# Optimization experiments

Hardware: AMD Instinct MI355X
Metric: run time of the kernel (lower is better)

Reference implementation:

```python
import jax, jax.numpy as jnp
import numpy as np

B, MQ, MK = 8, 512, 2048
Q_DIM, KV_DIM = 1024, 256
H = 8
QKC, VC = 1024, 1024
DQ, DV = QKC // H, VC // H
EPS = 1e-5  # nn.LayerNorm default


def _layer_norm(x, w, b):
    m = jnp.mean(x, axis=-1, keepdims=True)
    v = jnp.var(x, axis=-1, keepdims=True)
    return (x - m) * jax.lax.rsqrt(v + EPS) * w + b


def setup_inputs() -> dict:
    key = jax.random.key(0)
    ks = jax.random.split(key, 12)
    hidden_states = jax.random.normal(ks[0], (B, MQ, Q_DIM), dtype=jnp.float32)
    inputs = jax.random.normal(ks[1], (B, MK, KV_DIM), dtype=jnp.float32)
    # ragged per-batch kv lengths -> prefix-valid mask (matches keys[i, :n] packing)
    lengths = jax.random.randint(ks[2], (B,), MK // 4, MK + 1)
    inputs_mask = (jnp.arange(MK)[None, :] < lengths[:, None]).astype(jnp.int32)
    s = 0.02
    return {
        "hidden_states": hidden_states,
        "inputs": inputs,
        "inputs_mask": inputs_mask,
        "ln1_w": jnp.ones((Q_DIM,), jnp.float32),
        "ln1_b": jnp.zeros((Q_DIM,), jnp.float32),
        "ln2_w": jnp.ones((KV_DIM,), jnp.float32),
        "ln2_b": jnp.zeros((KV_DIM,), jnp.float32),
        "Wq": s * jax.random.normal(ks[3], (Q_DIM, QKC), dtype=jnp.float32),
        "bq": jnp.zeros((QKC,), jnp.float32),
        "Wk": s * jax.random.normal(ks[4], (KV_DIM, QKC), dtype=jnp.float32),
        "bk": jnp.zeros((QKC,), jnp.float32),
        "Wv": s * jax.random.normal(ks[5], (KV_DIM, VC), dtype=jnp.float32),
        "bv": jnp.zeros((VC,), jnp.float32),
    }


def reference(hidden_states, inputs, inputs_mask, ln1_w, ln1_b, ln2_w, ln2_b,
              Wq, bq, Wk, bk, Wv, bv):
    hs = _layer_norm(hidden_states, ln1_w, ln1_b)      # [B, MQ, Q_DIM]
    kv = _layer_norm(inputs, ln2_w, ln2_b)             # [B, MK, KV_DIM]

    q = (hs @ Wq + bq).reshape(B, MQ, H, DQ)           # [B, MQ, H, DQ]
    k = (kv @ Wk + bk).reshape(B, MK, H, DQ)           # [B, MK, H, DQ]
    v = (kv @ Wv + bv).reshape(B, MK, H, DV)           # [B, MK, H, DV]

    scores = jnp.einsum("bqhd,bkhd->bhqk", q, k) / jnp.sqrt(jnp.float32(DQ))
    mask_f = inputs_mask.astype(scores.dtype)          # [B, MK]
    neg = jnp.finfo(scores.dtype).min
    scores = scores + (1.0 - mask_f)[:, None, None, :] * neg
    probs = jax.nn.softmax(scores, axis=-1)            # [B, H, MQ, MK]

    ctx = jnp.einsum("bhqk,bkhd->bqhd", probs, v)      # [B, MQ, H, DV]
    return ctx.reshape(B, MQ, H * DV)
```

## Files before the change

kernel.cpp:

```cpp
#include <hip/hip_runtime.h>

#define DI __device__ __forceinline__

typedef _Float16 f16x8 __attribute__((ext_vector_type(8)));
typedef _Float16 f16x4 __attribute__((ext_vector_type(4)));
typedef float    f32x4 __attribute__((ext_vector_type(4)));

namespace {

constexpr int kB  = 8;
constexpr int kMQ = 512;
constexpr int kMK = 2048;
constexpr int kQKC = 1024;
constexpr int kVC  = 1024;

DI void gload16(const void* g, void* l) {
  __builtin_amdgcn_global_load_lds(
      (const __attribute__((address_space(1))) void*)g,
      (__attribute__((address_space(3))) void*)l, 16, 0, 0);
}

DI f32x4 mfma16(f16x8 a, f16x8 b, f32x4 c) {
  return __builtin_amdgcn_mfma_f32_16x16x32_f16(a, b, c, 0, 0, 0);
}

DI f32x4 mfma16k16(f16x4 a, f16x4 b, f32x4 c) {
  return __builtin_amdgcn_mfma_f32_16x16x16f16(a, b, c, 0, 0, 0);
}

template<int K, int N>
DI void transpose_dev(const float* __restrict__ W, _Float16* __restrict__ WT,
                      int bid, float (*t)[65]) {
  int nt = bid % (N / 64), kt = bid / (N / 64);
  int k0 = kt * 64, n0 = nt * 64;
  int tid = threadIdx.x;
#pragma unroll
  for (int j = 0; j < 16; ++j) {
    int e = tid + j * 256;
    int r = e >> 6, c = e & 63;
    t[r][c] = W[(size_t)(k0 + r) * N + n0 + c];
  }
  __syncthreads();
#pragma unroll
  for (int j = 0; j < 16; ++j) {
    int e = tid + j * 256;
    int r = e >> 6, c = e & 63;
    WT[(size_t)(n0 + r) * K + k0 + c] = (_Float16)t[c][r];
  }
}

DI void ln1024_dev(const float* __restrict__ x, const float* __restrict__ w,
                   const float* __restrict__ bb, _Float16* __restrict__ y,
                   int row, float* red) {
  int tid = threadIdx.x;
  const float4* xr = (const float4*)(x + (size_t)row * 1024);
  float4 v = xr[tid];
  float s = v.x + v.y + v.z + v.w;
  float q = v.x * v.x + v.y * v.y + v.z * v.z + v.w * v.w;
#pragma unroll
  for (int m = 32; m; m >>= 1) { s += __shfl_xor(s, m); q += __shfl_xor(q, m); }
  if ((tid & 63) == 0) { red[tid >> 6] = s; red[4 + (tid >> 6)] = q; }
  __syncthreads();
  s = red[0] + red[1] + red[2] + red[3];
  q = red[4] + red[5] + red[6] + red[7];
  float mean = s * (1.0f / 1024.0f);
  float var = q * (1.0f / 1024.0f) - mean * mean;
  float inv = rsqrtf(var + 1e-5f);
  f16x4 o;
  const float* wp = w + tid * 4;
  const float* bp = bb + tid * 4;
  o[0] = (_Float16)((v.x - mean) * inv * wp[0] + bp[0]);
  o[1] = (_Float16)((v.y - mean) * inv * wp[1] + bp[1]);
  o[2] = (_Float16)((v.z - mean) * inv * wp[2] + bp[2]);
  o[3] = (_Float16)((v.w - mean) * inv * wp[3] + bp[3]);
  *(f16x4*)(y + (size_t)row * 1024 + tid * 4) = o;
}

DI void ln256_dev(const float* __restrict__ x, const float* __restrict__ w,
                  const float* __restrict__ bb, _Float16* __restrict__ y, int bid) {
  int tid = threadIdx.x;
  int lane = tid & 63, wv = tid >> 6;
  size_t row = (size_t)bid * 4 + wv;
  const float4* xr = (const float4*)(x + row * 256);
  float4 v = xr[lane];
  float s = v.x + v.y + v.z + v.w;
  float q = v.x * v.x + v.y * v.y + v.z * v.z + v.w * v.w;
#pragma unroll
  for (int m = 32; m; m >>= 1) { s += __shfl_xor(s, m); q += __shfl_xor(q, m); }
  float mean = s * (1.0f / 256.0f);
  float var = q * (1.0f / 256.0f) - mean * mean;
  float inv = rsqrtf(var + 1e-5f);
  f16x4 o;
  const float* wp = w + lane * 4;
  const float* bp = bb + lane * 4;
  o[0] = (_Float16)((v.x - mean) * inv * wp[0] + bp[0]);
  o[1] = (_Float16)((v.y - mean) * inv * wp[1] + bp[1]);
  o[2] = (_Float16)((v.z - mean) * inv * wp[2] + bp[2]);
  o[3] = (_Float16)((v.w - mean) * inv * wp[3] + bp[3]);
  *(f16x4*)(y + row * 256 + lane * 4) = o;
}

__global__ __launch_bounds__(256) void prep_all(
    const float* __restrict__ Wq, const float* __restrict__ Wk, const float* __restrict__ Wv,
    _Float16* __restrict__ WqT, _Float16* __restrict__ WkT, _Float16* __restrict__ WvT,
    const float* __restrict__ hs, const float* __restrict__ ln1w, const float* __restrict__ ln1b,
    _Float16* __restrict__ hsln,
    const float* __restrict__ xin, const float* __restrict__ ln2w, const float* __restrict__ ln2b,
    _Float16* __restrict__ kvln) {
  __shared__ float tbuf[64][65];
  int bid = blockIdx.x;
  if (bid < 256) {
    transpose_dev<1024, 1024>(Wq, WqT, bid, tbuf);
  } else if (bid < 320) {
    transpose_dev<256, 1024>(Wk, WkT, bid - 256, tbuf);
  } else if (bid < 384) {
    transpose_dev<256, 1024>(Wv, WvT, bid - 320, tbuf);
  } else if (bid < 4480) {
    ln1024_dev(hs, ln1w, ln1b, hsln, bid - 384, (float*)tbuf);
  } else {
    ln256_dev(xin, ln2w, ln2b, kvln, bid - 4480);
  }
}

template<int M, int N, int K, bool BIAS_ROW, int MMODE, bool CM>
DI void gemm_dev(const _Float16* __restrict__ A, const _Float16* __restrict__ Bt,
                 const float* __restrict__ bias, const int* __restrict__ msk,
                 _Float16* __restrict__ C, int bid,
                 _Float16 (*As)[128 * 64], _Float16 (*Bs)[128 * 64]) {
  int tid = threadIdx.x, lane = tid & 63;
  int w = tid >> 6, wr = w >> 1, wc = w & 1;
  constexpr int NT = N / 128;
  constexpr int MT = M / 128;
  constexpr int KT = K / 64;
  int mt, nt;
  if constexpr (CM) { mt = bid % MT; nt = bid / MT; }
  else              { mt = bid / NT; nt = bid % NT; }
  if constexpr (MMODE == 1) { if (msk[mt * 128] == 0) return; }
  if constexpr (MMODE == 2) { if (msk[nt * 128] == 0) return; }
  const int l15 = lane & 15, l4 = lane >> 4;

  f32x4 acc[4][4] = {};

  const int rS = tid >> 3;
  const int cpS = tid & 7;

  auto stage = [&](int kt, int bufi) {
#pragma unroll
    for (int j = 0; j < 4; ++j) {
      int rr = rS + j * 32;
      int cg = cpS ^ (rr & 7);
      gload16(A  + ((size_t)(mt * 128 + rr) * K + kt * 64 + cg * 8),
              (char*)As[bufi] + j * 4096 + tid * 16);
      gload16(Bt + ((size_t)(nt * 128 + rr) * K + kt * 64 + cg * 8),
              (char*)Bs[bufi] + j * 4096 + tid * 16);
    }
  };

  stage(0, 0);
  __syncthreads();

  for (int kt = 0; kt < KT; ++kt) {
    int cur = kt & 1;
    if (kt + 1 < KT) stage(kt + 1, cur ^ 1);
#pragma unroll
    for (int ss = 0; ss < 2; ++ss) {
      f16x8 a[4], b[4];
#pragma unroll
      for (int m = 0; m < 4; ++m) {
        int ra = wr * 64 + m * 16 + l15;
        int cl = ss * 4 + l4;
        a[m] = *(const f16x8*)((const char*)As[cur] + ra * 128 + ((cl ^ (ra & 7)) << 4));
        int rb = wc * 64 + m * 16 + l15;
        b[m] = *(const f16x8*)((const char*)Bs[cur] + rb * 128 + ((cl ^ (rb & 7)) << 4));
      }
#pragma unroll
      for (int m = 0; m < 4; ++m)
#pragma unroll
        for (int n = 0; n < 4; ++n)
          acc[m][n] = mfma16(a[m], b[n], acc[m][n]);
    }
    __syncthreads();
  }

#pragma unroll
  for (int m = 0; m < 4; ++m) {
#pragma unroll
    for (int n = 0; n < 4; ++n) {
      int gi0 = mt * 128 + wr * 64 + m * 16 + l4 * 4;
      int gj  = nt * 128 + wc * 64 + n * 16 + l15;
#pragma unroll
      for (int r = 0; r < 4; ++r) {
        int gi = gi0 + r;
        float v = acc[m][n][r] + (BIAS_ROW ? bias[gi] : bias[gj]);
        C[(size_t)gi * N + gj] = (_Float16)v;
      }
    }
  }
}

__global__ __launch_bounds__(256) void gemm_all(
    const _Float16* __restrict__ hsln, const _Float16* __restrict__ WqT,
    const float* __restrict__ bq, _Float16* __restrict__ qbf,
    const _Float16* __restrict__ kvln, const _Float16* __restrict__ WkT,
    const float* __restrict__ bk, _Float16* __restrict__ kbf,
    const _Float16* __restrict__ WvT, const float* __restrict__ bv,
    _Float16* __restrict__ vT, const int* __restrict__ msk) {
  __shared__ _Float16 As[2][128 * 64];
  __shared__ _Float16 Bs[2][128 * 64];
  int bid = blockIdx.x;
  if (bid < 256) {
    gemm_dev<4096, 1024, 1024, false, 0, true>(hsln, WqT, bq, nullptr, qbf, bid, As, Bs);
  } else if (bid < 1280) {
    gemm_dev<16384, 1024, 256, false, 1, true>(kvln, WkT, bk, msk, kbf, bid - 256, As, Bs);
  } else {
    gemm_dev<1024, 16384, 256, true, 2, false>(WvT, kvln, bv, msk, vT, bid - 1280, As, Bs);
  }
}

__global__ __launch_bounds__(512, 4) void attn_kernel(const _Float16* __restrict__ qm,
                                                      const _Float16* __restrict__ km,
                                                      const _Float16* __restrict__ vT,
                                                      const int* __restrict__ msk,
                                                      float* __restrict__ out) {
  __shared__ _Float16 Ks[2][64 * 128];
  __shared__ _Float16 Vst[2][128 * 64];
  __shared__ float mlbuf[64][2];

  int tid = threadIdx.x, lane = tid & 63, w = tid >> 6;
  int bh = blockIdx.x & 63, qt = blockIdx.x >> 6;
  int h = bh & 7, b = bh >> 3;
  const int l15 = lane & 15, l4 = lane >> 4;
  const int wq = w & 3;
  const int g  = w >> 2;

  int vld = (lane < 32) ? msk[b * kMK + lane * 64] : 0;
  int ntiles = __popcll(__ballot(vld != 0));
  int lv = msk[b * kMK + (ntiles - 1) * 64 + lane];
  int lastlen = __popcll(__ballot(lv != 0));

  f16x8 qf[4];
#pragma unroll
  for (int kc = 0; kc < 4; ++kc)
    qf[kc] = *(const f16x8*)(qm +
        (size_t)(b * kMQ + qt * 64 + wq * 16 + l15) * kQKC +
        h * 128 + kc * 32 + l4 * 8);

  f32x4 o[8] = {};
  float rm = -1e30f, rl = 0.0f;

  const float sl2 = 0.08838834764831845f * 1.4426950408889634f;

  const int rK = tid >> 4, cpK = tid & 15;
  const int rV = tid >> 3, cpV = tid & 7;

  auto stage = [&](int kt, int bufi) {
#pragma unroll
    for (int j = 0; j < 2; ++j) {
      int rr = rK + j * 32;
      int cg = cpK ^ (rr & 7);
      gload16(km + (size_t)(b * kMK + kt * 64 + rr) * kQKC + h * 128 + cg * 8,
              (char*)Ks[bufi] + j * 8192 + tid * 16);
    }
#pragma unroll
    for (int j = 0; j < 2; ++j) {
      int dv = rV + j * 64;
      int cg = cpV ^ (dv & 7);
      gload16(vT + (size_t)(h * 128 + dv) * (kB * kMK) + (size_t)b * kMK + kt * 64 + cg * 8,
              (char*)Vst[bufi] + j * 8192 + tid * 16);
    }
  };

  stage(0, 0);
  __syncthreads();

  for (int kt = 0; kt < ntiles; ++kt) {
    int cur = kt & 1;
    if (kt + 1 < ntiles) stage(kt + 1, cur ^ 1);

    f32x4 sc[2] = {};
    __builtin_amdgcn_s_setprio(1);
#pragma unroll
    for (int kc = 0; kc < 4; ++kc) {
      f16x8 kb[2];
#pragma unroll
      for (int kf = 0; kf < 2; ++kf) {
        int rr = g * 32 + kf * 16 + l15;
        int cl = kc * 4 + l4;
        kb[kf] = *(const f16x8*)((const char*)Ks[cur] + rr * 256 + ((cl ^ (rr & 7)) << 4));
      }
#pragma unroll
      for (int kf = 0; kf < 2; ++kf)
        sc[kf] = mfma16(kb[kf], qf[kc], sc[kf]);
    }
    __builtin_amdgcn_s_setprio(0);

    if (kt == ntiles - 1) {
#pragma unroll
      for (int kf = 0; kf < 2; ++kf)
#pragma unroll
        for (int r = 0; r < 4; ++r)
          if (g * 32 + kf * 16 + l4 * 4 + r >= lastlen) sc[kf][r] = -3e38f;
    }

    float mx = sc[0][0];
#pragma unroll
    for (int kf = 0; kf < 2; ++kf)
#pragma unroll
      for (int r = 0; r < 4; ++r) mx = fmaxf(mx, sc[kf][r]);
    mx = fmaxf(mx, __shfl_xor(mx, 16));
    mx = fmaxf(mx, __shfl_xor(mx, 32));
    float al = 1.0f;
    if (__any(mx > rm)) {
      float nm = fmaxf(rm, mx);
      al = __builtin_amdgcn_exp2f((rm - nm) * sl2);
      rm = nm;
#pragma unroll
      for (int n = 0; n < 8; ++n)
#pragma unroll
        for (int r = 0; r < 4; ++r) o[n][r] *= al;
    }
    float nms = rm * sl2;
    float ts = 0.0f;
#pragma unroll
    for (int kf = 0; kf < 2; ++kf)
#pragma unroll
      for (int r = 0; r < 4; ++r) {
        float p = __builtin_amdgcn_exp2f(sc[kf][r] * sl2 - nms);
        sc[kf][r] = p;
        ts += p;
      }
    ts += __shfl_xor(ts, 16);
    ts += __shfl_xor(ts, 32);
    rl = rl * al + ts;

    f16x4 pb[2];
#pragma unroll
    for (int kf = 0; kf < 2; ++kf)
#pragma unroll
      for (int r = 0; r < 4; ++r) pb[kf][r] = (_Float16)sc[kf][r];

    __builtin_amdgcn_s_setprio(1);
#pragma unroll
    for (int n = 0; n < 8; ++n) {
      int dv = n * 16 + l15;
#pragma unroll
      for (int kf = 0; kf < 2; ++kf) {
        int phys = (g * 4 + kf * 2 + (l4 >> 1)) ^ (dv & 7);
        f16x4 vb = *(const f16x4*)((const char*)Vst[cur] +
                                   dv * 128 + (phys << 4) + (l4 & 1) * 8);
        o[n] = mfma16k16(vb, pb[kf], o[n]);
      }
    }
    __builtin_amdgcn_s_setprio(0);
    __syncthreads();
  }

  float* Mbuf = (float*)Ks;
  if (g == 1) {
#pragma unroll
    for (int n = 0; n < 8; ++n)
#pragma unroll
      for (int r = 0; r < 4; ++r)
        Mbuf[(n * 16 + l4 * 4 + r) * 64 + wq * 16 + l15] = o[n][r];
    if (l4 == 0) {
      mlbuf[wq * 16 + l15][0] = rm;
      mlbuf[wq * 16 + l15][1] = rl;
    }
  }
  __syncthreads();
  if (g == 1) return;

  float m1 = mlbuf[wq * 16 + l15][0];
  float l1 = mlbuf[wq * 16 + l15][1];
  float m = fmaxf(rm, m1);
  float w0 = __builtin_amdgcn_exp2f((rm - m) * sl2);
  float w1 = __builtin_amdgcn_exp2f((m1 - m) * sl2);
  float inv = 1.0f / (rl * w0 + l1 * w1);
  w0 *= inv; w1 *= inv;

  int qg = qt * 64 + wq * 16 + l15;
#pragma unroll
  for (int n = 0; n < 8; ++n) {
    f32x4 ov;
#pragma unroll
    for (int r = 0; r < 4; ++r) {
      float o1 = Mbuf[(n * 16 + l4 * 4 + r) * 64 + wq * 16 + l15];
      ov[r] = o[n][r] * w0 + o1 * w1;
    }
    *(f32x4*)(out + ((size_t)b * kMQ + qg) * kVC + h * 128 + n * 16 + l4 * 4) = ov;
  }
}

}

extern "C" void kernel_launch(void* const* d_in, const int* in_sizes, int n_in,
                              void* d_out, int out_size, void* d_ws, size_t ws_size,
                              hipStream_t stream) {
  (void)in_sizes; (void)n_in; (void)out_size; (void)ws_size;
  const float* hs   = (const float*)d_in[0];
  const float* xin  = (const float*)d_in[1];
  const int*   msk  = (const int*)d_in[2];
  const float* ln1w = (const float*)d_in[3];
  const float* ln1b = (const float*)d_in[4];
  const float* ln2w = (const float*)d_in[5];
  const float* ln2b = (const float*)d_in[6];
  const float* Wq   = (const float*)d_in[7];
  const float* bq   = (const float*)d_in[8];
  const float* Wk   = (const float*)d_in[9];
  const float* bk   = (const float*)d_in[10];
  const float* Wv   = (const float*)d_in[11];
  const float* bv   = (const float*)d_in[12];
  float* out = (float*)d_out;

  char* ws = (char*)d_ws;
  _Float16* qbf  = (_Float16*)(ws + 0);
  _Float16* kbf  = (_Float16*)(ws + 8388608);
  _Float16* vT   = (_Float16*)(ws + 41943040);
  _Float16* hsln = (_Float16*)(ws + 75497472);
  _Float16* kvln = (_Float16*)(ws + 83886080);
  _Float16* WqT  = (_Float16*)(ws + 92274688);
  _Float16* WkT  = (_Float16*)(ws + 94371840);
  _Float16* WvT  = (_Float16*)(ws + 94896128);

  prep_all<<<8576, 256, 0, stream>>>(Wq, Wk, Wv, WqT, WkT, WvT,
                                     hs, ln1w, ln1b, hsln,
                                     xin, ln2w, ln2b, kvln);
  gemm_all<<<2304, 256, 0, stream>>>(hsln, WqT, bq, qbf,
                                     kvln, WkT, bk, kbf,
                                     WvT, bv, vT, msk);
  attn_kernel<<<512, 512, 0, stream>>>(qbf, kbf, vT, msk, out);
}
```

Before: 122.0 us.

## Process two 16-row query fragments per wave to reuse K/V tiles

Each attention block now handles 128 query rows instead of 64, with every wave holding two query fragments and running two sets of MFMAs against each K and V fragment read from shared memory. This halves the total K/V global traffic and LDS reads per output, and halves the grid to 256 blocks. In exchange it doubles the accumulator registers, lowers the occupancy bound to 2 blocks per CU, and leaves fewer blocks than the device's CU count, which risks idle CUs and a worse load balance across ragged kv lengths.

Measured after the change: 116.2 us. 1.05x faster.

```diff
diff --git a/kernel.cpp b/kernel.cpp
--- a/kernel.cpp
+++ b/kernel.cpp
@@ -217,14 +217,15 @@
   }
 }
 
-__global__ __launch_bounds__(512, 4) void attn_kernel(const _Float16* __restrict__ qm,
+__global__ __launch_bounds__(512, 2) void attn_kernel(const _Float16* __restrict__ qm,
                                                       const _Float16* __restrict__ km,
                                                       const _Float16* __restrict__ vT,
                                                       const int* __restrict__ msk,
                                                       float* __restrict__ out) {
-  __shared__ _Float16 Ks[2][64 * 128];
-  __shared__ _Float16 Vst[2][128 * 64];
-  __shared__ float mlbuf[64][2];
+  __shared__ __align__(16) char smem[66560];
+  _Float16* Ksp = (_Float16*)smem;
+  _Float16* Vsp = (_Float16*)(smem + 32768);
+  float*    mlb = (float*)(smem + 65536);
 
   int tid = threadIdx.x, lane = tid & 63, w = tid >> 6;
   int bh = blockIdx.x & 63, qt = blockIdx.x >> 6;
@@ -238,15 +239,17 @@
   int lv = msk[b * kMK + (ntiles - 1) * 64 + lane];
   int lastlen = __popcll(__ballot(lv != 0));
 
-  f16x8 qf[4];
-#pragma unroll
-  for (int kc = 0; kc < 4; ++kc)
-    qf[kc] = *(const f16x8*)(qm +
-        (size_t)(b * kMQ + qt * 64 + wq * 16 + l15) * kQKC +
-        h * 128 + kc * 32 + l4 * 8);
-
-  f32x4 o[8] = {};
-  float rm = -1e30f, rl = 0.0f;
+  f16x8 qf[2][4];
+#pragma unroll
+  for (int m = 0; m < 2; ++m)
+#pragma unroll
+    for (int kc = 0; kc < 4; ++kc)
+      qf[m][kc] = *(const f16x8*)(qm +
+          (size_t)(b * kMQ + qt * 128 + wq * 32 + m * 16 + l15) * kQKC +
+          h * 128 + kc * 32 + l4 * 8);
+
+  f32x4 o[2][8] = {};
+  float rm[2] = {-1e30f, -1e30f}, rl[2] = {0.0f, 0.0f};
 
   const float sl2 = 0.08838834764831845f * 1.4426950408889634f;
 
@@ -259,14 +262,14 @@
       int rr = rK + j * 32;
       int cg = cpK ^ (rr & 7);
       gload16(km + (size_t)(b * kMK + kt * 64 + rr) * kQKC + h * 128 + cg * 8,
-              (char*)Ks[bufi] + j * 8192 + tid * 16);
+              (char*)Ksp + bufi * 16384 + j * 8192 + tid * 16);
     }
 #pragma unroll
     for (int j = 0; j < 2; ++j) {
       int dv = rV + j * 64;
       int cg = cpV ^ (dv & 7);
       gload16(vT + (size_t)(h * 128 + dv) * (kB * kMK) + (size_t)b * kMK + kt * 64 + cg * 8,
-              (char*)Vst[bufi] + j * 8192 + tid * 16);
+              (char*)Vsp + bufi * 16384 + j * 8192 + tid * 16);
     }
   };
 
@@ -277,7 +280,7 @@
     int cur = kt & 1;
     if (kt + 1 < ntiles) stage(kt + 1, cur ^ 1);
 
-    f32x4 sc[2] = {};
+    f32x4 sc[2][2] = {};
     __builtin_amdgcn_s_setprio(1);
 #pragma unroll
     for (int kc = 0; kc < 4; ++kc) {
@@ -286,58 +289,70 @@
       for (int kf = 0; kf < 2; ++kf) {
         int rr = g * 32 + kf * 16 + l15;
         int cl = kc * 4 + l4;
-        kb[kf] = *(const f16x8*)((const char*)Ks[cur] + rr * 256 + ((cl ^ (rr & 7)) << 4));
-      }
+        kb[kf] = *(const f16x8*)((const char*)Ksp + cur * 16384 + rr * 256 +
+                                 ((cl ^ (rr & 7)) << 4));
+      }
+#pragma unroll
+      for (int m = 0; m < 2; ++m)
+#pragma unroll
+        for (int kf = 0; kf < 2; ++kf)
+          sc[m][kf] = mfma16(kb[kf], qf[m][kc], sc[m][kf]);
+    }
+    __builtin_amdgcn_s_setprio(0);
+
+    if (kt == ntiles - 1) {
 #pragma unroll
       for (int kf = 0; kf < 2; ++kf)
-        sc[kf] = mfma16(kb[kf], qf[kc], sc[kf]);
-    }
-    __builtin_amdgcn_s_setprio(0);
-
-    if (kt == ntiles - 1) {
+#pragma unroll
+        for (int r = 0; r < 4; ++r)
+          if (g * 32 + kf * 16 + l4 * 4 + r >= lastlen) {
+            sc[0][kf][r] = -3e38f;
+            sc[1][kf][r] = -3e38f;
+          }
+    }
+
+    float mx[2];
+#pragma unroll
+    for (int m = 0; m < 2; ++m) {
+      float v = sc[m][0][0];
 #pragma unroll
       for (int kf = 0; kf < 2; ++kf)
 #pragma unroll
-        for (int r = 0; r < 4; ++r)
-          if (g * 32 + kf * 16 + l4 * 4 + r >= lastlen) sc[kf][r] = -3e38f;
-    }
-
-    float mx = sc[0][0];
-#pragma unroll
-    for (int kf = 0; kf < 2; ++kf)
-#pragma unroll
-      for (int r = 0; r < 4; ++r) mx = fmaxf(mx, sc[kf][r]);
-    mx = fmaxf(mx, __shfl_xor(mx, 16));
-    mx = fmaxf(mx, __shfl_xor(mx, 32));
-    float al = 1.0f;
-    if (__any(mx > rm)) {
-      float nm = fmaxf(rm, mx);
-      al = __builtin_amdgcn_exp2f((rm - nm) * sl2);
-      rm = nm;
-#pragma unroll
-      for (int n = 0; n < 8; ++n)
-#pragma unroll
-        for (int r = 0; r < 4; ++r) o[n][r] *= al;
-    }
-    float nms = rm * sl2;
-    float ts = 0.0f;
-#pragma unroll
-    for (int kf = 0; kf < 2; ++kf)
-#pragma unroll
-      for (int r = 0; r < 4; ++r) {
-        float p = __builtin_amdgcn_exp2f(sc[kf][r] * sl2 - nms);
-        sc[kf][r] = p;
-        ts += p;
-      }
-    ts += __shfl_xor(ts, 16);
-    ts += __shfl_xor(ts, 32);
-    rl = rl * al + ts;
-
-    f16x4 pb[2];
-#pragma unroll
-    for (int kf = 0; kf < 2; ++kf)
-#pragma unroll
-      for (int r = 0; r < 4; ++r) pb[kf][r] = (_Float16)sc[kf][r];
+        for (int r = 0; r < 4; ++r) v = fmaxf(v, sc[m][kf][r]);
+      v = fmaxf(v, __shfl_xor(v, 16));
+      v = fmaxf(v, __shfl_xor(v, 32));
+      mx[m] = v;
+    }
+    float al[2] = {1.0f, 1.0f};
+    if (__any(mx[0] > rm[0] || mx[1] > rm[1])) {
+#pragma unroll
+      for (int m = 0; m < 2; ++m) {
+        float nm = fmaxf(rm[m], mx[m]);
+        al[m] = __builtin_amdgcn_exp2f((rm[m] - nm) * sl2);
+        rm[m] = nm;
+#pragma unroll
+        for (int n = 0; n < 8; ++n)
+#pragma unroll
+          for (int r = 0; r < 4; ++r) o[m][n][r] *= al[m];
+      }
+    }
+    f16x4 pb[2][2];
+#pragma unroll
+    for (int m = 0; m < 2; ++m) {
+      float nms = rm[m] * sl2;
+      float ts = 0.0f;
+#pragma unroll
+      for (int kf = 0; kf < 2; ++kf)
+#pragma unroll
+        for (int r = 0; r < 4; ++r) {
+          float p = __builtin_amdgcn_exp2f(sc[m][kf][r] * sl2 - nms);
+          pb[m][kf][r] = (_Float16)p;
+          ts += p;
+        }
+      ts += __shfl_xor(ts, 16);
+      ts += __shfl_xor(ts, 32);
+      rl[m] = rl[m] * al[m] + ts;
+    }
 
     __builtin_amdgcn_s_setprio(1);
 #pragma unroll
@@ -346,48 +361,56 @@
 #pragma unroll
       for (int kf = 0; kf < 2; ++kf) {
         int phys = (g * 4 + kf * 2 + (l4 >> 1)) ^ (dv & 7);
-        f16x4 vb = *(const f16x4*)((const char*)Vst[cur] +
+        f16x4 vb = *(const f16x4*)((const char*)Vsp + cur * 16384 +
                                    dv * 128 + (phys << 4) + (l4 & 1) * 8);
-        o[n] = mfma16k16(vb, pb[kf], o[n]);
+#pragma unroll
+        for (int m = 0; m < 2; ++m)
+          o[m][n] = mfma16k16(vb, pb[m][kf], o[m][n]);
       }
     }
     __builtin_amdgcn_s_setprio(0);
     __syncthreads();
   }
 
-  float* Mbuf = (float*)Ks;
+  float* Mbuf = (float*)smem;
   if (g == 1) {
 #pragma unroll
-    for (int n = 0; n < 8; ++n)
-#pragma unroll
-      for (int r = 0; r < 4; ++r)
-        Mbuf[(n * 16 + l4 * 4 + r) * 64 + wq * 16 + l15] = o[n][r];
-    if (l4 == 0) {
-      mlbuf[wq * 16 + l15][0] = rm;
-      mlbuf[wq * 16 + l15][1] = rl;
+    for (int m = 0; m < 2; ++m) {
+#pragma unroll
+      for (int n = 0; n < 8; ++n)
+#pragma unroll
+        for (int r = 0; r < 4; ++r)
+          Mbuf[(n * 16 + l4 * 4 + r) * 128 + wq * 32 + m * 16 + l15] = o[m][n][r];
+      if (l4 == 0) {
+        mlb[(wq * 32 + m * 16 + l15) * 2 + 0] = rm[m];
+        mlb[(wq * 32 + m * 16 + l15) * 2 + 1] = rl[m];
+      }
     }
   }
   __syncthreads();
   if (g == 1) return;
 
-  float m1 = mlbuf[wq * 16 + l15][0];
-  float l1 = mlbuf[wq * 16 + l15][1];
-  float m = fmaxf(rm, m1);
-  float w0 = __builtin_amdgcn_exp2f((rm - m) * sl2);
-  float w1 = __builtin_amdgcn_exp2f((m1 - m) * sl2);
-  float inv = 1.0f / (rl * w0 + l1 * w1);
-  w0 *= inv; w1 *= inv;
-
-  int qg = qt * 64 + wq * 16 + l15;
-#pragma unroll
-  for (int n = 0; n < 8; ++n) {
-    f32x4 ov;
-#pragma unroll
-    for (int r = 0; r < 4; ++r) {
-      float o1 = Mbuf[(n * 16 + l4 * 4 + r) * 64 + wq * 16 + l15];
-      ov[r] = o[n][r] * w0 + o1 * w1;
-    }
-    *(f32x4*)(out + ((size_t)b * kMQ + qg) * kVC + h * 128 + n * 16 + l4 * 4) = ov;
+#pragma unroll
+  for (int m = 0; m < 2; ++m) {
+    int ql = wq * 32 + m * 16 + l15;
+    float m1 = mlb[ql * 2 + 0];
+    float l1 = mlb[ql * 2 + 1];
+    float mm = fmaxf(rm[m], m1);
+    float w0 = __builtin_amdgcn_exp2f((rm[m] - mm) * sl2);
+    float w1 = __builtin_amdgcn_exp2f((m1 - mm) * sl2);
+    float inv = 1.0f / (rl[m] * w0 + l1 * w1);
+    w0 *= inv; w1 *= inv;
+    int qg = qt * 128 + ql;
+#pragma unroll
+    for (int n = 0; n < 8; ++n) {
+      f32x4 ov;
+#pragma unroll
+      for (int r = 0; r < 4; ++r) {
+        float o1 = Mbuf[(n * 16 + l4 * 4 + r) * 128 + ql];
+        ov[r] = o[m][n][r] * w0 + o1 * w1;
+      }
+      *(f32x4*)(out + ((size_t)b * kMQ + qg) * kVC + h * 128 + n * 16 + l4 * 4) = ov;
+    }
   }
 }
 
@@ -428,5 +451,5 @@
   gemm_all<<<2304, 256, 0, stream>>>(hsln, WqT, bq, qbf,
                                      kvln, WkT, bk, kbf,
                                      WvT, bv, vT, msk);
-  attn_kernel<<<512, 512, 0, stream>>>(qbf, kbf, vT, msk, out);
-}
+  attn_kernel<<<256, 512, 0, stream>>>(qbf, kbf, vT, msk, out);
+}
```

## Balance ragged attention work by pairing long and short batches per block

Applied to the files above, without the earlier changes.

The attention kernel now launches 256 blocks instead of 512. Each block processes two (batch, q-tile) work items for its head: it ranks the batches by number of valid KV tiles and pairs the rank-pc batch with the rank-(7-pc) batch. This evens out per-block work under ragged sequence lengths and reduces tail imbalance. The costs are fewer concurrent blocks, with launch bounds lowered to 2 per SIMD, and items within a block running serially with extra syncs.

New measurement: 133.6 us. 9.5% more time.

```diff
diff --git a/kernel.cpp b/kernel.cpp
--- a/kernel.cpp
+++ b/kernel.cpp
@@ -217,177 +217,206 @@
   }
 }
 
-__global__ __launch_bounds__(512, 4) void attn_kernel(const _Float16* __restrict__ qm,
+__global__ __launch_bounds__(512, 2) void attn_kernel(const _Float16* __restrict__ qm,
                                                       const _Float16* __restrict__ km,
                                                       const _Float16* __restrict__ vT,
                                                       const int* __restrict__ msk,
                                                       float* __restrict__ out) {
-  __shared__ _Float16 Ks[2][64 * 128];
-  __shared__ _Float16 Vst[2][128 * 64];
-  __shared__ float mlbuf[64][2];
+  __shared__ _Float16 Ksp[2][64 * 128];
+  __shared__ _Float16 Vsp[2][128 * 64];
+  __shared__ float mlb[64][2];
 
   int tid = threadIdx.x, lane = tid & 63, w = tid >> 6;
-  int bh = blockIdx.x & 63, qt = blockIdx.x >> 6;
-  int h = bh & 7, b = bh >> 3;
   const int l15 = lane & 15, l4 = lane >> 4;
   const int wq = w & 3;
   const int g  = w >> 2;
 
-  int vld = (lane < 32) ? msk[b * kMK + lane * 64] : 0;
-  int ntiles = __popcll(__ballot(vld != 0));
-  int lv = msk[b * kMK + (ntiles - 1) * 64 + lane];
-  int lastlen = __popcll(__ballot(lv != 0));
-
-  f16x8 qf[4];
-#pragma unroll
-  for (int kc = 0; kc < 4; ++kc)
-    qf[kc] = *(const f16x8*)(qm +
-        (size_t)(b * kMQ + qt * 64 + wq * 16 + l15) * kQKC +
-        h * 128 + kc * 32 + l4 * 8);
-
-  f32x4 o[8] = {};
-  float rm = -1e30f, rl = 0.0f;
+  const int c  = blockIdx.x & 7;
+  const int m  = blockIdx.x >> 3;
+  const int pc = m >> 3;
+  const int s  = m & 7;
+  const int h  = c;
+
+  int nt0, nt1, nt2, nt3, nt4, nt5, nt6, nt7;
+  {
+    int nts[8];
+#pragma unroll
+    for (int bb = 0; bb < 8; ++bb) {
+      int vld = (lane < 32) ? msk[bb * kMK + lane * 64] : 0;
+      nts[bb] = __popcll(__ballot(vld != 0));
+    }
+    nt0 = nts[0]; nt1 = nts[1]; nt2 = nts[2]; nt3 = nts[3];
+    nt4 = nts[4]; nt5 = nts[5]; nt6 = nts[6]; nt7 = nts[7];
+  }
+  int bA = 0, bB = 0, ntA = 0, ntB = 0;
+  {
+    int nts[8] = {nt0, nt1, nt2, nt3, nt4, nt5, nt6, nt7};
+#pragma unroll
+    for (int bb = 0; bb < 8; ++bb) {
+      int rk = 0;
+#pragma unroll
+      for (int j = 0; j < 8; ++j)
+        rk += (nts[j] > nts[bb]) || (nts[j] == nts[bb] && j < bb);
+      if (rk == pc)     { bA = bb; ntA = nts[bb]; }
+      if (rk == 7 - pc) { bB = bb; ntB = nts[bb]; }
+    }
+  }
 
   const float sl2 = 0.08838834764831845f * 1.4426950408889634f;
 
   const int rK = tid >> 4, cpK = tid & 15;
   const int rV = tid >> 3, cpV = tid & 7;
 
-  auto stage = [&](int kt, int bufi) {
-#pragma unroll
-    for (int j = 0; j < 2; ++j) {
-      int rr = rK + j * 32;
-      int cg = cpK ^ (rr & 7);
-      gload16(km + (size_t)(b * kMK + kt * 64 + rr) * kQKC + h * 128 + cg * 8,
-              (char*)Ks[bufi] + j * 8192 + tid * 16);
-    }
-#pragma unroll
-    for (int j = 0; j < 2; ++j) {
-      int dv = rV + j * 64;
-      int cg = cpV ^ (dv & 7);
-      gload16(vT + (size_t)(h * 128 + dv) * (kB * kMK) + (size_t)b * kMK + kt * 64 + cg * 8,
-              (char*)Vst[bufi] + j * 8192 + tid * 16);
-    }
-  };
-
-  stage(0, 0);
-  __syncthreads();
-
-  for (int kt = 0; kt < ntiles; ++kt) {
-    int cur = kt & 1;
-    if (kt + 1 < ntiles) stage(kt + 1, cur ^ 1);
-
-    f32x4 sc[2] = {};
-    __builtin_amdgcn_s_setprio(1);
-#pragma unroll
-    for (int kc = 0; kc < 4; ++kc) {
-      f16x8 kb[2];
-#pragma unroll
-      for (int kf = 0; kf < 2; ++kf) {
-        int rr = g * 32 + kf * 16 + l15;
-        int cl = kc * 4 + l4;
-        kb[kf] = *(const f16x8*)((const char*)Ks[cur] + rr * 256 + ((cl ^ (rr & 7)) << 4));
-      }
+#pragma unroll 1
+  for (int it = 0; it < 2; ++it) {
+    const int b = it == 0 ? bA : bB;
+    const int ntiles = it == 0 ? ntA : ntB;
+    const int qt = s;
+
+    int lv = msk[b * kMK + (ntiles - 1) * 64 + lane];
+    int lastlen = __popcll(__ballot(lv != 0));
+
+    f16x8 qf[4];
+#pragma unroll
+    for (int kc = 0; kc < 4; ++kc)
+      qf[kc] = *(const f16x8*)(qm +
+          (size_t)(b * kMQ + qt * 64 + wq * 16 + l15) * kQKC +
+          h * 128 + kc * 32 + l4 * 8);
+
+    f32x4 o[8] = {};
+    float rm = -1e30f, rl = 0.0f;
+
+    auto stage = [&](int kt, int bufi) {
+#pragma unroll
+      for (int j = 0; j < 2; ++j) {
+        int rr = rK + j * 32;
+        int cg = cpK ^ (rr & 7);
+        gload16(km + (size_t)(b * kMK + kt * 64 + rr) * kQKC + h * 128 + cg * 8,
+                (char*)Ksp[bufi] + j * 8192 + tid * 16);
+      }
+#pragma unroll
+      for (int j = 0; j < 2; ++j) {
+        int dv = rV + j * 64;
+        int cg = cpV ^ (dv & 7);
+        gload16(vT + (size_t)(h * 128 + dv) * (kB * kMK) + (size_t)b * kMK + kt * 64 + cg * 8,
+                (char*)Vsp[bufi] + j * 8192 + tid * 16);
+      }
+    };
+
+    __syncthreads();
+    stage(0, 0);
+    __syncthreads();
+
+    for (int kt = 0; kt < ntiles; ++kt) {
+      int cur = kt & 1;
+      if (kt + 1 < ntiles) stage(kt + 1, cur ^ 1);
+
+      f32x4 sc[2] = {};
+      __builtin_amdgcn_s_setprio(1);
+#pragma unroll
+      for (int kc = 0; kc < 4; ++kc) {
+        f16x8 kb[2];
+#pragma unroll
+        for (int kf = 0; kf < 2; ++kf) {
+          int rr = g * 32 + kf * 16 + l15;
+          int cl = kc * 4 + l4;
+          kb[kf] = *(const f16x8*)((const char*)Ksp[cur] + rr * 256 + ((cl ^ (rr & 7)) << 4));
+        }
+#pragma unroll
+        for (int kf = 0; kf < 2; ++kf)
+          sc[kf] = mfma16(kb[kf], qf[kc], sc[kf]);
+      }
+      __builtin_amdgcn_s_setprio(0);
+
+      if (kt == ntiles - 1) {
+#pragma unroll
+        for (int kf = 0; kf < 2; ++kf)
+#pragma unroll
+          for (int r = 0; r < 4; ++r)
+            if (g * 32 + kf * 16 + l4 * 4 + r >= lastlen) sc[kf][r] = -3e38f;
+      }
+
+      float mx = sc[0][0];
 #pragma unroll
       for (int kf = 0; kf < 2; ++kf)
-        sc[kf] = mfma16(kb[kf], qf[kc], sc[kf]);
-    }
-    __builtin_amdgcn_s_setprio(0);
-
-    if (kt == ntiles - 1) {
+#pragma unroll
+        for (int r = 0; r < 4; ++r) mx = fmaxf(mx, sc[kf][r]);
+      mx = fmaxf(mx, __shfl_xor(mx, 16));
+      mx = fmaxf(mx, __shfl_xor(mx, 32));
+      float al = 1.0f;
+      if (__any(mx > rm)) {
+        float nm = fmaxf(rm, mx);
+        al = __builtin_amdgcn_exp2f((rm - nm) * sl2);
+        rm = nm;
+#pragma unroll
+        for (int n = 0; n < 8; ++n)
+#pragma unroll
+          for (int r = 0; r < 4; ++r) o[n][r] *= al;
+      }
+      float nms = rm * sl2;
+      float ts = 0.0f;
+      f16x4 pb[2];
 #pragma unroll
       for (int kf = 0; kf < 2; ++kf)
 #pragma unroll
+        for (int r = 0; r < 4; ++r) {
+          float p = __builtin_amdgcn_exp2f(sc[kf][r] * sl2 - nms);
+          pb[kf][r] = (_Float16)p;
+          ts += p;
+        }
+      ts += __shfl_xor(ts, 16);
+      ts += __shfl_xor(ts, 32);
+      rl = rl * al + ts;
+
+      __builtin_amdgcn_s_setprio(1);
+#pragma unroll
+      for (int n = 0; n < 8; ++n) {
+        int dv = n * 16 + l15;
+#pragma unroll
+        for (int kf = 0; kf < 2; ++kf) {
+          int phys = (g * 4 + kf * 2 + (l4 >> 1)) ^ (dv & 7);
+          f16x4 vb = *(const f16x4*)((const char*)Vsp[cur] +
+                                     dv * 128 + (phys << 4) + (l4 & 1) * 8);
+          o[n] = mfma16k16(vb, pb[kf], o[n]);
+        }
+      }
+      __builtin_amdgcn_s_setprio(0);
+      __syncthreads();
+    }
+
+    float* Mbuf = (float*)Ksp;
+    if (g == 1) {
+#pragma unroll
+      for (int n = 0; n < 8; ++n)
+#pragma unroll
         for (int r = 0; r < 4; ++r)
-          if (g * 32 + kf * 16 + l4 * 4 + r >= lastlen) sc[kf][r] = -3e38f;
-    }
-
-    float mx = sc[0][0];
-#pragma unroll
-    for (int kf = 0; kf < 2; ++kf)
-#pragma unroll
-      for (int r = 0; r < 4; ++r) mx = fmaxf(mx, sc[kf][r]);
-    mx = fmaxf(mx, __shfl_xor(mx, 16));
-    mx = fmaxf(mx, __shfl_xor(mx, 32));
-    float al = 1.0f;
-    if (__any(mx > rm)) {
-      float nm = fmaxf(rm, mx);
-      al = __builtin_amdgcn_exp2f((rm - nm) * sl2);
-      rm = nm;
-#pragma unroll
-      for (int n = 0; n < 8; ++n)
-#pragma unroll
-        for (int r = 0; r < 4; ++r) o[n][r] *= al;
-    }
-    float nms = rm * sl2;
-    float ts = 0.0f;
-#pragma unroll
-    for (int kf = 0; kf < 2; ++kf)
-#pragma unroll
-      for (int r = 0; r < 4; ++r) {
-        float p = __builtin_amdgcn_exp2f(sc[kf][r] * sl2 - nms);
-        sc[kf][r] = p;
-        ts += p;
-      }
-    ts += __shfl_xor(ts, 16);
-    ts += __shfl_xor(ts, 32);
-    rl = rl * al + ts;
-
-    f16x4 pb[2];
-#pragma unroll
-    for (int kf = 0; kf < 2; ++kf)
-#pragma unroll
-      for (int r = 0; r < 4; ++r) pb[kf][r] = (_Float16)sc[kf][r];
-
-    __builtin_amdgcn_s_setprio(1);
-#pragma unroll
-    for (int n = 0; n < 8; ++n) {
-      int dv = n * 16 + l15;
-#pragma unroll
-      for (int kf = 0; kf < 2; ++kf) {
-        int phys = (g * 4 + kf * 2 + (l4 >> 1)) ^ (dv & 7);
-        f16x4 vb = *(const f16x4*)((const char*)Vst[cur] +
-                                   dv * 128 + (phys << 4) + (l4 & 1) * 8);
-        o[n] = mfma16k16(vb, pb[kf], o[n]);
-      }
-    }
-    __builtin_amdgcn_s_setprio(0);
+          Mbuf[(n * 16 + l4 * 4 + r) * 64 + wq * 16 + l15] = o[n][r];
+      if (l4 == 0) {
+        mlb[wq * 16 + l15][0] = rm;
+        mlb[wq * 16 + l15][1] = rl;
+      }
+    }
     __syncthreads();
-  }
-
-  float* Mbuf = (float*)Ks;
-  if (g == 1) {
-#pragma unroll
-    for (int n = 0; n < 8; ++n)
-#pragma unroll
-      for (int r = 0; r < 4; ++r)
-        Mbuf[(n * 16 + l4 * 4 + r) * 64 + wq * 16 + l15] = o[n][r];
-    if (l4 == 0) {
-      mlbuf[wq * 16 + l15][0] = rm;
-      mlbuf[wq * 16 + l15][1] = rl;
-    }
-  }
-  __syncthreads();
-  if (g == 1) return;
-
-  float m1 = mlbuf[wq * 16 + l15][0];
-  float l1 = mlbuf[wq * 16 + l15][1];
-  float m = fmaxf(rm, m1);
-  float w0 = __builtin_amdgcn_exp2f((rm - m) * sl2);
-  float w1 = __builtin_amdgcn_exp2f((m1 - m) * sl2);
-  float inv = 1.0f / (rl * w0 + l1 * w1);
-  w0 *= inv; w1 *= inv;
-
-  int qg = qt * 64 + wq * 16 + l15;
-#pragma unroll
-  for (int n = 0; n < 8; ++n) {
-    f32x4 ov;
-#pragma unroll
-    for (int r = 0; r < 4; ++r) {
-      float o1 = Mbuf[(n * 16 + l4 * 4 + r) * 64 + wq * 16 + l15];
-      ov[r] = o[n][r] * w0 + o1 * w1;
-    }
-    *(f32x4*)(out + ((size_t)b * kMQ + qg) * kVC + h * 128 + n * 16 + l4 * 4) = ov;
+    if (g == 0) {
+      float m1 = mlb[wq * 16 + l15][0];
+      float l1 = mlb[wq * 16 + l15][1];
+      float mm = fmaxf(rm, m1);
+      float w0 = __builtin_amdgcn_exp2f((rm - mm) * sl2);
+      float w1 = __builtin_amdgcn_exp2f((m1 - mm) * sl2);
+      float inv = 1.0f / (rl * w0 + l1 * w1);
+      w0 *= inv; w1 *= inv;
+      int qg = qt * 64 + wq * 16 + l15;
+#pragma unroll
+      for (int n = 0; n < 8; ++n) {
+        f32x4 ov;
+#pragma unroll
+        for (int r = 0; r < 4; ++r) {
+          float o1 = Mbuf[(n * 16 + l4 * 4 + r) * 64 + wq * 16 + l15];
+          ov[r] = o[n][r] * w0 + o1 * w1;
+        }
+        *(f32x4*)(out + ((size_t)b * kMQ + qg) * kVC + h * 128 + n * 16 + l4 * 4) = ov;
+      }
+    }
   }
 }
 
@@ -428,5 +457,5 @@
   gemm_all<<<2304, 256, 0, stream>>>(hsln, WqT, bq, qbf,
                                      kvln, WkT, bk, kbf,
                                      WvT, bv, vT, msk);
-  attn_kernel<<<512, 512, 0, stream>>>(qbf, kbf, vT, msk, out);
-}
+  attn_kernel<<<256, 512, 0, stream>>>(qbf, kbf, vT, msk, out);
+}
```
